# Optimization experiments

Measured on AMD Instinct MI355X. Metric: run time of the kernel, lower is better.

The kernel has to match this reference:

```python
import jax, jax.numpy as jnp
import numpy as np

EPS_L2 = 1e-6
EPS_RMS = 1e-6

def _dw_causal(x, w):
    # depthwise causal conv: x [B,L,C], w [C,K] (torch Conv1d weight [C,1,K] squeezed)
    K = w.shape[1]
    L = x.shape[1]
    xp = jnp.pad(x, ((0, 0), (K - 1, 0), (0, 0)))
    out = jnp.zeros_like(x)
    for j in range(K):  # K=4, fixed small kernel
        out = out + w[:, j] * xp[:, j:j + L, :]
    return out

def _qkv_conv(x, dw, pw):
    # depthwise causal conv -> pointwise 1x1 conv -> SiLU
    return jax.nn.silu(_dw_causal(x, dw) @ pw.T)

def _l2n(x):
    return x / (jnp.linalg.norm(x, axis=-1, keepdims=True) + EPS_L2)

def setup_inputs() -> dict:
    key = jax.random.key(0)
    B, L, D, M, P, K = 2, 1024, 2048, 2048, 8, 4
    ks = jax.random.split(key, 16)
    inp = {}
    inp['x'] = jax.random.normal(ks[0], (B, L, D), dtype=jnp.float32)
    inp['Wq'] = jax.random.normal(ks[1], (M, D), dtype=jnp.float32) * 0.02
    inp['Wk'] = jax.random.normal(ks[2], (M, D), dtype=jnp.float32) * 0.02
    inp['Wv'] = jax.random.normal(ks[3], (M, D), dtype=jnp.float32) * 0.02
    inp['q_dw'] = jax.random.normal(ks[4], (M, K), dtype=jnp.float32) * 0.1
    inp['k_dw'] = jax.random.normal(ks[5], (M, K), dtype=jnp.float32) * 0.1
    inp['v_dw'] = jax.random.normal(ks[6], (M, K), dtype=jnp.float32) * 0.1
    inp['q_pw'] = jax.random.normal(ks[7], (M, M), dtype=jnp.float32) * 0.02
    inp['k_pw'] = jax.random.normal(ks[8], (M, M), dtype=jnp.float32) * 0.02
    inp['v_pw'] = jax.random.normal(ks[9], (M, M), dtype=jnp.float32) * 0.02
    inp['pk'] = jax.random.normal(ks[10], (P, M), dtype=jnp.float32) * 0.02
    inp['pv'] = jax.random.normal(ks[11], (P, M), dtype=jnp.float32) * 0.02
    inp['mlp_w1'] = jnp.eye(M, dtype=jnp.float32) * 0.1
    inp['mlp_w2'] = jnp.eye(M, dtype=jnp.float32) * 0.1
    inp['eta_w'] = jnp.zeros((1, D), dtype=jnp.float32)
    inp['eta_b'] = jnp.full((1,), 2.0, dtype=jnp.float32)
    inp['theta_w'] = jnp.zeros((1, D), dtype=jnp.float32)
    inp['theta_b'] = jnp.full((1,), -1.0, dtype=jnp.float32)
    inp['alpha_w'] = jnp.zeros((1, D), dtype=jnp.float32)
    inp['alpha_b'] = jnp.full((1,), -2.0, dtype=jnp.float32)
    inp['gate_w'] = jax.random.normal(ks[12], (M, M), dtype=jnp.float32) * 0.02
    inp['gate_b'] = jnp.zeros((M,), dtype=jnp.float32)
    inp['out_w'] = jax.random.normal(ks[13], (D, M), dtype=jnp.float32) * 0.02
    inp['ln_w'] = jnp.ones((D,), dtype=jnp.float32)
    inp['mem_state'] = jnp.zeros((M, M), dtype=jnp.float32)
    inp['sur_state'] = jnp.zeros((M, M), dtype=jnp.float32)
    return inp

def reference(x, Wq, Wk, Wv, q_dw, q_pw, k_dw, k_pw, v_dw, v_pw, pk, pv,
              mlp_w1, mlp_w2, eta_w, eta_b, theta_w, theta_b, alpha_w, alpha_b,
              gate_w, gate_b, out_w, ln_w, mem_state, sur_state):
    B, L, D = x.shape
    M = Wq.shape[0]
    P = pk.shape[0]
    # projections + causal depthwise-separable convs + SiLU
    q = _qkv_conv(x @ Wq.T, q_dw, q_pw)
    k = _qkv_conv(x @ Wk.T, k_dw, k_pw)
    v = _qkv_conv(x @ Wv.T, v_dw, v_pw)
    q = _l2n(q)
    k = _l2n(k)
    # data-dependent eta/theta/alpha from mean-pooled input, scalarized
    x_pooled = x.mean(axis=1)  # [B, D]
    eta = jax.nn.sigmoid(x_pooled @ eta_w.T + eta_b).mean()
    theta = jax.nn.sigmoid(x_pooled @ theta_w.T + theta_b).mean()
    alpha = jax.nn.sigmoid(x_pooled @ alpha_w.T + alpha_b).mean()
    # persistent memory tokens
    pk_n = _l2n(pk)
    k_wp = jnp.concatenate([jnp.broadcast_to(pk_n[None], (B, P, M)), k], axis=1)
    v_wp = jnp.concatenate([jnp.broadcast_to(pv[None], (B, P, M)), v], axis=1)
    # test-time memory update (torch.no_grad block -> stop_gradient)
    pred = jnp.einsum('blm,mh->blh', k, mem_state)
    err = v - pred
    momentary = jnp.einsum('bld,blh->dh', k, err) / (B * L)
    new_surprise = eta * sur_state + theta * momentary
    new_memory = (1.0 - alpha) * mem_state + new_surprise
    snapshot = jax.lax.stop_gradient(new_memory)
    # retrieval: linear memory + deep memory MLP
    linear_ret = jnp.einsum('blm,mh->blh', q, snapshot)
    mlp_ret = jax.nn.silu(q @ mlp_w1.T) @ mlp_w2.T
    retrieved = linear_ret + mlp_ret
    # causal attention with always-visible persistent tokens
    scores = jnp.einsum('blm,bpm->blp', q, k_wp) / jnp.sqrt(jnp.float32(M))
    col = jnp.arange(P + L)
    row = jnp.arange(L)
    mask = (col[None, :] < P) | ((col[None, :] - P) <= row[:, None])  # [L, P+L]
    scores = jnp.where(mask[None], scores, -jnp.inf)
    attn = jax.nn.softmax(scores.astype(jnp.float32), axis=-1).astype(x.dtype)
    context = jnp.einsum('blp,bpm->blm', attn, v_wp)
    retrieved = retrieved + context
    # gated output projection + residual + RMSNorm
    gate = jax.nn.sigmoid(retrieved @ gate_w.T + gate_b)
    out = x + (gate * retrieved) @ out_w.T
    rms = jnp.sqrt(jnp.mean(out * out, axis=-1, keepdims=True) + EPS_RMS)
    return (out / rms) * ln_w
```

## Files before the change

### kernel.cpp

```cpp
#include <hip/hip_runtime.h>
#include <hip/hip_bf16.h>


#define NROWS 2048
#define MD    2048
#define PL    1032
#define PLP   1152
#define NM    4194304

using bf16x8 = __attribute__((ext_vector_type(8))) __bf16;
using f32x4  = __attribute__((ext_vector_type(4))) float;
using u16x8  = __attribute__((ext_vector_type(8))) unsigned short;

__device__ __forceinline__ unsigned short f2bf(float f) {
    union { float f; unsigned int u; } c; c.f = f;
    unsigned int u = c.u;
    return (unsigned short)((u + 0x7fffu + ((u >> 16) & 1u)) >> 16);
}
__device__ __forceinline__ float bf2f(unsigned short h) {
    union { float f; unsigned int u; } c; c.u = ((unsigned int)h) << 16;
    return c.f;
}
__device__ __forceinline__ float ldf(const float* p) { return *p; }
__device__ __forceinline__ float ldf(const unsigned short* p) { return bf2f(*p); }
__device__ __forceinline__ float sigm(float x) { return 1.f / (1.f + __expf(-x)); }
__device__ __forceinline__ float silu(float x) { return x / (1.f + __expf(-x)); }

__device__ __forceinline__ float block_reduce_sum(float v) {
    __shared__ float ws[4];
    #pragma unroll
    for (int o = 32; o > 0; o >>= 1) v += __shfl_down(v, o);
    __syncthreads();
    if ((threadIdx.x & 63) == 0) ws[threadIdx.x >> 6] = v;
    __syncthreads();
    return (ws[0] + ws[1]) + (ws[2] + ws[3]);
}
__device__ __forceinline__ float block_reduce_max(float v) {
    __shared__ float wm[4];
    #pragma unroll
    for (int o = 32; o > 0; o >>= 1) v = fmaxf(v, __shfl_down(v, o));
    __syncthreads();
    if ((threadIdx.x & 63) == 0) wm[threadIdx.x >> 6] = v;
    __syncthreads();
    return fmaxf(fmaxf(wm[0], wm[1]), fmaxf(wm[2], wm[3]));
}

__device__ __forceinline__ void load_lds16(const unsigned short* g, unsigned short* l) {
    __builtin_amdgcn_global_load_lds(
        (const __attribute__((address_space(1))) unsigned int*)g,
        (__attribute__((address_space(3))) unsigned int*)l, 16, 0, 0);
}
__device__ __forceinline__ void raw_barrier() {
    __asm__ volatile("" ::: "memory");
    __builtin_amdgcn_s_barrier();
    __asm__ volatile("" ::: "memory");
}
__device__ __forceinline__ void swz_bid(int& bx, int& by, int& bz) {
    const int gx = gridDim.x, gy = gridDim.y, gz = gridDim.z;
    const int nwg = gx * gy * gz;
    int id = blockIdx.x + gx * (blockIdx.y + gy * blockIdx.z);
    if ((nwg & 7) == 0) { int c = nwg >> 3; id = (id & 7) * c + (id >> 3); }
    bx = id % gx; id /= gx; by = id % gy; bz = id / gy;
}
__device__ __forceinline__ void epi_store(int epi, float* Cf, unsigned short* Ch,
                                          long off, int gc, float v,
                                          const float* gbp, const float* r1z,
                                          const float* r2z, unsigned short* qhz) {
    if (epi == 0)      Cf[off] = v;
    else if (epi == 1) Cf[off] += v;
    else if (epi == 2) Ch[off] = f2bf(v);
    else if (epi == 3) Ch[off] = f2bf(silu(v));
    else if (epi == 4) Ch[off] = f2bf(sigm(v + gbp[gc]) * (r1z[off] + r2z[off]));
    else { float r = Cf[off] + v; Cf[off] = r; qhz[off] = f2bf(r + r2z[off]); }
}

__global__ __launch_bounds__(256) void gemm_nt(
    const unsigned short* __restrict__ A, const unsigned short* __restrict__ Bm,
    void* __restrict__ Cv, int Mc, int K, long sA, long sB, long sCb, int epiPack,
    const float* __restrict__ gbp, const float* __restrict__ r1,
    const float* __restrict__ r2, unsigned short* __restrict__ qh)
{
    __shared__ unsigned short As[2][8192];
    __shared__ unsigned short Bs[2][4096];
    int bxx, byy, bzz; swz_bid(bxx, byy, bzz);
    const int tid = threadIdx.x, lane = tid & 63, w = tid >> 6;
    const int l16 = lane & 15, quad = lane >> 4;
    const int wr = (w >> 1) * 64, wc = (w & 1) * 32;
    const long rowBase = (long)byy * 128;
    const long colBase = (long)bxx * 64;
    const unsigned short* Ap = A + (long)bzz * sA;
    const unsigned short* Bp = Bm + (long)bzz * sB;
    const int epi = (epiPack >> (bzz * 4)) & 15;
    const int r8 = lane >> 3;
    const int cg = (lane & 7) ^ r8;

    const unsigned short* gA[4]; const unsigned short* gB[2];
    unsigned short* lA[4]; unsigned short* lB[2];
    #pragma unroll
    for (int t = 0; t < 4; ++t) {
        int ch = w * 4 + t;
        gA[t] = Ap + (rowBase + ch * 8 + r8) * (long)K + cg * 8;
        lA[t] = &As[0][ch * 512];
    }
    #pragma unroll
    for (int t = 0; t < 2; ++t) {
        int ch = w * 2 + t;
        gB[t] = Bp + (colBase + ch * 8 + r8) * (long)K + cg * 8;
        lB[t] = &Bs[0][ch * 512];
    }

    f32x4 acc[4][2] = {};
    #pragma unroll
    for (int t = 0; t < 4; ++t) { load_lds16(gA[t], lA[t]); gA[t] += 64; }
    #pragma unroll
    for (int t = 0; t < 2; ++t) { load_lds16(gB[t], lB[t]); gB[t] += 64; }

    const int nIter = K >> 6;
    for (int it = 0; it < nIter; ++it) {
        const int cb = it & 1;
        if (it + 1 < nIter) {
            const int nb = cb ^ 1;
            #pragma unroll
            for (int t = 0; t < 4; ++t) { load_lds16(gA[t], lA[t] + nb * 8192); gA[t] += 64; }
            #pragma unroll
            for (int t = 0; t < 2; ++t) { load_lds16(gB[t], lB[t] + nb * 4096); gB[t] += 64; }
            __builtin_amdgcn_s_waitcnt(0xF76);
        } else {
            __builtin_amdgcn_s_waitcnt(0xF70);
        }
        raw_barrier();
        const unsigned short* Ac = As[cb];
        const unsigned short* Bc = Bs[cb];
        #pragma unroll
        for (int ks = 0; ks < 2; ++ks) {
            const int cl = ((ks * 4 + quad) ^ (l16 & 7)) * 8;
            bf16x8 af[4], bfr[2];
            #pragma unroll
            for (int i = 0; i < 4; ++i)
                af[i] = *(const bf16x8*)&Ac[(wr + i * 16 + l16) * 64 + cl];
            #pragma unroll
            for (int j = 0; j < 2; ++j)
                bfr[j] = *(const bf16x8*)&Bc[(wc + j * 16 + l16) * 64 + cl];
            #pragma unroll
            for (int i = 0; i < 4; ++i)
                #pragma unroll
                for (int j = 0; j < 2; ++j)
                    acc[i][j] = __builtin_amdgcn_mfma_f32_16x16x32_bf16(af[i], bfr[j], acc[i][j], 0, 0, 0);
        }
        raw_barrier();
    }

    char* Cb = (char*)Cv + (long)bzz * sCb;
    float* Cf = (float*)Cb;
    unsigned short* Ch = (unsigned short*)Cb;
    const long zel = (long)bzz * (sCb >> 2);
    const float* r1z = r1 + zel;
    const float* r2z = r2 + zel;
    unsigned short* qhz = qh + zel;
    #pragma unroll
    for (int i = 0; i < 4; ++i)
        #pragma unroll
        for (int r = 0; r < 4; ++r) {
            long gr = rowBase + wr + i * 16 + quad * 4 + r;
            #pragma unroll
            for (int j = 0; j < 2; ++j) {
                long gc = colBase + wc + j * 16 + l16;
                epi_store(epi, Cf, Ch, gr * (long)Mc + gc, (int)gc, acc[i][j][r],
                          gbp, r1z, r2z, qhz);
            }
        }
}

#define P8_RD_A(p)                                                              \
    _Pragma("unroll") for (int fr = 0; fr < 2; ++fr)                            \
    _Pragma("unroll") for (int ks = 0; ks < 2; ++ks)                            \
        af[fr][ks] = *(const bf16x8*)&Ac[(wr + ((p) * 2 + fr) * 16 + l16) * 64  \
                                         + ((ks * 4 + quad) ^ (l16 & 7)) * 8];
#define P8_MFMA(p)                                                              \
    __builtin_amdgcn_s_setprio(1);                                              \
    _Pragma("unroll") for (int ks = 0; ks < 2; ++ks)                            \
    _Pragma("unroll") for (int fr = 0; fr < 2; ++fr)                            \
    _Pragma("unroll") for (int fc = 0; fc < FC; ++fc)                           \
        acc[(p) * 2 + fr][fc] = __builtin_amdgcn_mfma_f32_16x16x32_bf16(        \
            af[fr][ks], bfr[fc][ks], acc[(p) * 2 + fr][fc], 0, 0, 0);           \
    __builtin_amdgcn_s_setprio(0);
#define P8_STG_A(h)                                                             \
    do { load_lds16(gA[h][0], &Anx[lofsA[h][0]]); gA[h][0] += 64;               \
         load_lds16(gA[h][1], &Anx[lofsA[h][1]]); gA[h][1] += 64; } while (0)
#define P8_STG_B(j)                                                             \
    do { load_lds16(gB[j], &Bnx[lofsB[j]]); gB[j] += 64; } while (0)

template <int BN>
__global__ __launch_bounds__(512, 2) void gemm_nt_8p(
    const unsigned short* __restrict__ A, const unsigned short* __restrict__ Bm,
    void* __restrict__ Cv, int Mc, int K, long sA, long sB, long sCb, int epiPack,
    const unsigned short* __restrict__ rh)
{
    constexpr int LB = BN / 64;
    constexpr int FC = BN / 64;
    constexpr int WN = BN / 4;
    __shared__ unsigned short As[2][16384];
    __shared__ unsigned short Bs[2][BN * 64];
    int bx, by, bz; swz_bid(bx, by, bz);
    const int tid = threadIdx.x, lane = tid & 63, w = tid >> 6;
    const int l16 = lane & 15, quad = lane >> 4;
    const int wr = (w >> 2) * 128, wc = (w & 3) * WN;
    const long rowBase = (long)by * 256;
    const long colBase = (long)bx * BN;
    const unsigned short* Ap = A + (long)bz * sA;
    const unsigned short* Bp = Bm + (long)bz * sB;
    const int epi = (epiPack >> (bz * 4)) & 15;
    const int r8 = lane >> 3;
    const int cg = (lane & 7) ^ r8;

    const unsigned short* gA[2][2];
    int lofsA[2][2];
    #pragma unroll
    for (int h = 0; h < 2; ++h)
        #pragma unroll
        for (int j = 0; j < 2; ++j) {
            const int rowOff = h * 128 + j * 64 + w * 8 + r8;
            gA[h][j] = Ap + (rowBase + rowOff) * (long)K + cg * 8;
            lofsA[h][j] = (h * 128 + j * 64 + w * 8) * 64;
        }
    const unsigned short* gB[LB];
    int lofsB[LB];
    #pragma unroll
    for (int j = 0; j < LB; ++j) {
        const int rowOff = j * 64 + w * 8 + r8;
        gB[j] = Bp + (colBase + rowOff) * (long)K + cg * 8;
        lofsB[j] = (j * 64 + w * 8) * 64;
    }

    const int nT = K >> 6;
    f32x4 acc[8][FC] = {};

    #pragma unroll
    for (int h = 0; h < 2; ++h)
        #pragma unroll
        for (int j = 0; j < 2; ++j) { load_lds16(gA[h][j], &As[0][lofsA[h][j]]); gA[h][j] += 64; }
    #pragma unroll
    for (int j = 0; j < LB; ++j) { load_lds16(gB[j], &Bs[0][lofsB[j]]); gB[j] += 64; }
    if (nT > 1) {
        #pragma unroll
        for (int j = 0; j < LB; ++j) { load_lds16(gB[j], &Bs[1][lofsB[j]]); gB[j] += 64; }
        __builtin_amdgcn_s_waitcnt(0x0F70 | LB);
    } else {
        __builtin_amdgcn_s_waitcnt(0x0F70);
    }
    raw_barrier();

    for (int t = 0; t < nT; ++t) {
        const int cb = t & 1;
        const unsigned short* Ac = As[cb];
        const unsigned short* Bc = Bs[cb];
        unsigned short* Anx = As[cb ^ 1];
        unsigned short* Bnx = Bs[cb];
        const bool stA = (t + 1 < nT);
        const bool stB = (t + 2 < nT);
        bf16x8 bfr[FC][2];
        bf16x8 af[2][2];

        #pragma unroll
        for (int fc = 0; fc < FC; ++fc)
            #pragma unroll
            for (int ks = 0; ks < 2; ++ks)
                bfr[fc][ks] = *(const bf16x8*)&Bc[(wc + fc * 16 + l16) * 64
                                                 + ((ks * 4 + quad) ^ (l16 & 7)) * 8];
        P8_RD_A(0)
        if (stA) P8_STG_A(0);
        raw_barrier();
        P8_MFMA(0)
        raw_barrier();

        P8_RD_A(1)
        if (stA) P8_STG_A(1);
        raw_barrier();
        P8_MFMA(1)
        raw_barrier();

        P8_RD_A(2)
        if (stB) {
            #pragma unroll
            for (int j = 0; j < (LB + 1) / 2; ++j) P8_STG_B(j);
        }
        raw_barrier();
        P8_MFMA(2)
        raw_barrier();

        P8_RD_A(3)
        if (stB) {
            #pragma unroll
            for (int j = (LB + 1) / 2; j < LB; ++j) P8_STG_B(j);
            __builtin_amdgcn_s_waitcnt(0x0F70 | LB);
        } else {
            __builtin_amdgcn_s_waitcnt(0x0F70);
        }
        raw_barrier();
        P8_MFMA(3)
        raw_barrier();
    }

    char* Cb = (char*)Cv + (long)bz * sCb;
    float* Cf = (float*)Cb;
    unsigned short* Ch = (unsigned short*)Cb;
    #pragma unroll
    for (int i = 0; i < 8; ++i)
        #pragma unroll
        for (int r = 0; r < 4; ++r) {
            long gr = rowBase + wr + i * 16 + quad * 4 + r;
            #pragma unroll
            for (int j = 0; j < FC; ++j) {
                long gc = colBase + wc + j * 16 + l16;
                long off = gr * (long)Mc + gc;
                float v = acc[i][j][r];
                if (epi == 0)      Cf[off] = v;
                else if (epi == 2) Ch[off] = f2bf(v);
                else if (epi == 3) Ch[off] = f2bf(silu(v));
                else               Ch[off] = f2bf(bf2f(rh[off]) - v);
            }
        }
}

template <typename TS>
__global__ void k_transpose(const TS* __restrict__ src, unsigned short* __restrict__ dst,
                            int R, int C, int dstLd, int dstOff, long sSrc, long sDst)
{
    __shared__ float tile[32][33];
    const TS* sp = src + (long)blockIdx.z * sSrc;
    unsigned short* dp = dst + (long)blockIdx.z * sDst;
    int c0 = blockIdx.x * 32, r0 = blockIdx.y * 32;
    int tx = threadIdx.x, ty = threadIdx.y;
    #pragma unroll
    for (int i = 0; i < 4; ++i)
        tile[ty + i * 8][tx] = ldf(&sp[(long)(r0 + ty + i * 8) * C + c0 + tx]);
    __syncthreads();
    #pragma unroll
    for (int i = 0; i < 4; ++i)
        dp[(long)(c0 + ty + i * 8) * dstLd + dstOff + r0 + tx] = f2bf(tile[tx][ty + i * 8]);
}

__global__ void k_errT_kT(const unsigned short* __restrict__ errN,
                          const unsigned short* __restrict__ k_bf, unsigned short* __restrict__ eT)
{
    __shared__ float tile[32][33];
    int z = blockIdx.z;
    const unsigned short* src = (z == 0) ? errN : k_bf;
    int c0 = blockIdx.x * 32, r0 = blockIdx.y * 32;
    int tx = threadIdx.x, ty = threadIdx.y;
    #pragma unroll
    for (int i = 0; i < 4; ++i) {
        long idx = (long)(r0 + ty + i * 8) * MD + c0 + tx;
        tile[ty + i * 8][tx] = bf2f(src[idx]);
    }
    __syncthreads();
    unsigned short* dst = eT + (long)z * NM;
    #pragma unroll
    for (int i = 0; i < 4; ++i)
        dst[(long)(c0 + ty + i * 8) * MD + r0 + tx] = f2bf(tile[tx][ty + i * 8]);
}

__global__ void k_snapT(const float* __restrict__ mem, const float* __restrict__ sur,
                        const float* __restrict__ momT, const float* __restrict__ scal,
                        unsigned short* __restrict__ dst)
{
    __shared__ float tile[32][33];
    float eta = scal[0], theta = scal[1], alpha = scal[2];
    int h0 = blockIdx.y * 32, d0 = blockIdx.x * 32;
    int tx = threadIdx.x, ty = threadIdx.y;
    #pragma unroll
    for (int i = 0; i < 4; ++i) {
        long idx = (long)(d0 + ty + i * 8) * MD + h0 + tx;
        tile[ty + i * 8][tx] = (1.f - alpha) * mem[idx] + eta * sur[idx];
    }
    __syncthreads();
    #pragma unroll
    for (int i = 0; i < 4; ++i) {
        long oidx = (long)(h0 + ty + i * 8) * MD + d0 + tx;
        dst[oidx] = f2bf(tile[tx][ty + i * 8] + theta * (1.f / 2048.f) * momT[oidx]);
    }
}

__global__ void k_cvt_multi(const float* s0, const float* s1, const float* s2, const float* s3,
                            const float* s4, const float* s5, const float* s6, const float* s7,
                            unsigned short* d0, unsigned short* d1, unsigned short* d2, unsigned short* d3,
                            unsigned short* d4, unsigned short* d5, unsigned short* d6, unsigned short* d7)
{
    int seg = blockIdx.x >> 11;
    const float* s; unsigned short* d;
    switch (seg) {
        case 0: s = s0; d = d0; break;  case 1: s = s1; d = d1; break;
        case 2: s = s2; d = d2; break;  case 3: s = s3; d = d3; break;
        case 4: s = s4; d = d4; break;  case 5: s = s5; d = d5; break;
        case 6: s = s6; d = d6; break;  default: s = s7; d = d7; break;
    }
    long idx = ((long)(blockIdx.x & 2047) * 256 + threadIdx.x) * 8;
    float4 a = *(const float4*)(s + idx);
    float4 b = *(const float4*)(s + idx + 4);
    u16x8 o;
    o[0] = f2bf(a.x); o[1] = f2bf(a.y); o[2] = f2bf(a.z); o[3] = f2bf(a.w);
    o[4] = f2bf(b.x); o[5] = f2bf(b.y); o[6] = f2bf(b.z); o[7] = f2bf(b.w);
    *(u16x8*)(d + idx) = o;
}

__global__ void k_dwconv(const unsigned short* __restrict__ tproj,
                         const float* __restrict__ qdw, const float* __restrict__ kdw,
                         const float* __restrict__ vdw, unsigned short* __restrict__ conv)
{
    long u = (long)blockIdx.x * 256 + threadIdx.x;
    long flat = u * 8;
    int z = (int)(flat >> 22);
    int rem = (int)(flat & (NM - 1));
    int n = rem >> 11, m = rem & 2047;
    int l = n & 1023;
    const float* dw = (z == 0) ? qdw : (z == 1) ? kdw : vdw;
    const unsigned short* src = tproj + (long)n * 6144 + z * 2048 + m;
    float4 dwv[8];
    #pragma unroll
    for (int e = 0; e < 8; ++e) dwv[e] = *(const float4*)(dw + (m + e) * 4);
    float acc[8] = {};
    #pragma unroll
    for (int j = 0; j < 4; ++j) {
        int dl = j - 3;
        if (l + dl >= 0) {
            u16x8 r = *(const u16x8*)(src + (long)dl * 6144);
            #pragma unroll
            for (int e = 0; e < 8; ++e)
                acc[e] += ((const float*)&dwv[e])[j] * bf2f(r[e]);
        }
    }
    u16x8 o;
    #pragma unroll
    for (int e = 0; e < 8; ++e) o[e] = f2bf(acc[e]);
    *(u16x8*)(conv + (long)z * NM + (long)n * 2048 + m) = o;
}

__global__ void k_post_qkv(const unsigned short* __restrict__ tbf, unsigned short* __restrict__ q_bf,
                           unsigned short* __restrict__ k_bf, unsigned short* __restrict__ kwp)
{
    int bid = blockIdx.x, z = bid >> 11, n = bid & 2047;
    const unsigned short* row = tbf + (long)z * NM + (long)n * 2048;
    int t = threadIdx.x;
    u16x8 iv = *(const u16x8*)(row + t * 8);
    float v[8];
    #pragma unroll
    for (int e = 0; e < 8; ++e) v[e] = bf2f(iv[e]);
    float ss = 0.f;
    #pragma unroll
    for (int e = 0; e < 8; ++e) ss += v[e] * v[e];
    ss = block_reduce_sum(ss);
    float inv = 1.f / (sqrtf(ss) + 1e-6f);
    u16x8 o;
    #pragma unroll
    for (int e = 0; e < 8; ++e) o[e] = f2bf(v[e] * inv);
    if (z == 0) {
        *(u16x8*)(q_bf + (long)n * 2048 + t * 8) = o;
    } else {
        *(u16x8*)(k_bf + (long)n * 2048 + t * 8) = o;
        int bb = n >> 10, l = n & 1023;
        *(u16x8*)(kwp + ((long)bb * PLP + 8 + l) * MD + t * 8) = o;
    }
}

__global__ void k_misc(const float* __restrict__ pk, const float* __restrict__ pv,
                       unsigned short* __restrict__ kwp, unsigned short* __restrict__ vwpT)
{
    int bid = blockIdx.x, t = threadIdx.x;
    if (bid < 8) {
        const float* row = pk + bid * MD;
        float4 a = *(const float4*)(row + t * 8);
        float4 b = *(const float4*)(row + t * 8 + 4);
        float v[8] = {a.x, a.y, a.z, a.w, b.x, b.y, b.z, b.w};
        float ss = 0.f;
        #pragma unroll
        for (int e = 0; e < 8; ++e) ss += v[e] * v[e];
        ss = block_reduce_sum(ss);
        float inv = 1.f / (sqrtf(ss) + 1e-6f);
        u16x8 o;
        #pragma unroll
        for (int e = 0; e < 8; ++e) o[e] = f2bf(v[e] * inv);
        *(u16x8*)(kwp + (long)bid * MD + t * 8) = o;
        *(u16x8*)(kwp + (long)PLP * MD + (long)bid * MD + t * 8) = o;
    } else if (bid < 72) {
        int i = (bid - 8) * 256 + t;
        int m = i >> 3, pp = i & 7;
        unsigned short h = f2bf(pv[pp * MD + m]);
        vwpT[(long)m * PLP + pp] = h;
        vwpT[(long)MD * PLP + (long)m * PLP + pp] = h;
    } else if (bid < 312) {
        long flat = ((long)(bid - 72) * 256 + t) * 8;
        int b = (int)(flat / 245760);
        int r = (int)(flat % 245760);
        int j = 1032 + (r >> 11), m = r & 2047;
        u16x8 zz = {};
        *(u16x8*)(kwp + ((long)b * PLP + j) * MD + m) = zz;
    } else {
        long flat = ((long)(bid - 312) * 256 + t) * 8;
        int bm = (int)(flat / 120);
        int o = (int)(flat % 120);
        u16x8 zz = {};
        *(u16x8*)(vwpT + (long)bm * PLP + 1032 + o) = zz;
    }
}

__global__ void k_pooled(const float* __restrict__ x, const float* __restrict__ ew,
                         const float* __restrict__ tw, const float* __restrict__ aw,
                         float* __restrict__ dots, unsigned short* __restrict__ xbf) {
    int b = blockIdx.y;
    long flat = ((long)blockIdx.x * 256 + threadIdx.x) * 8;
    long gi = (long)b * 1024 * MD + flat;
    int d = (int)(flat & (MD - 1));
    float4 a = *(const float4*)(x + gi);
    float4 b4 = *(const float4*)(x + gi + 4);
    float xv[8] = {a.x, a.y, a.z, a.w, b4.x, b4.y, b4.z, b4.w};
    float4 e0 = *(const float4*)(ew + d), e1 = *(const float4*)(ew + d + 4);
    float4 t0 = *(const float4*)(tw + d), t1 = *(const float4*)(tw + d + 4);
    float4 w0 = *(const float4*)(aw + d), w1 = *(const float4*)(aw + d + 4);
    u16x8 o;
    #pragma unroll
    for (int e = 0; e < 8; ++e) o[e] = f2bf(xv[e]);
    *(u16x8*)(xbf + gi) = o;
    float s0 = xv[0]*e0.x + xv[1]*e0.y + xv[2]*e0.z + xv[3]*e0.w
             + xv[4]*e1.x + xv[5]*e1.y + xv[6]*e1.z + xv[7]*e1.w;
    float s1 = xv[0]*t0.x + xv[1]*t0.y + xv[2]*t0.z + xv[3]*t0.w
             + xv[4]*t1.x + xv[5]*t1.y + xv[6]*t1.z + xv[7]*t1.w;
    float s2 = xv[0]*w0.x + xv[1]*w0.y + xv[2]*w0.z + xv[3]*w0.w
             + xv[4]*w1.x + xv[5]*w1.y + xv[6]*w1.z + xv[7]*w1.w;
    s0 = block_reduce_sum(s0);
    if (threadIdx.x == 0) atomicAdd(&dots[0 + b], s0);
    s1 = block_reduce_sum(s1);
    if (threadIdx.x == 0) atomicAdd(&dots[2 + b], s1);
    s2 = block_reduce_sum(s2);
    if (threadIdx.x == 0) atomicAdd(&dots[4 + b], s2);
}
__global__ void k_scal_fin(const float* __restrict__ dots, const float* __restrict__ eb,
                           const float* __restrict__ tb, const float* __restrict__ ab,
                           float* __restrict__ scal) {
    if (threadIdx.x == 0 && blockIdx.x == 0) {
        const float invL = 1.f / 1024.f;
        float e = 0, th = 0, al = 0;
        for (int b = 0; b < 2; ++b) {
            e  += sigm(dots[0 + b] * invL + eb[0]);
            th += sigm(dots[2 + b] * invL + tb[0]);
            al += sigm(dots[4 + b] * invL + ab[0]);
        }
        scal[0] = e * 0.5f; scal[1] = th * 0.5f; scal[2] = al * 0.5f;
    }
}

__global__ void k_softmax(const float* __restrict__ S, unsigned short* __restrict__ attn) {
    int l = blockIdx.x, b = blockIdx.y;
    long base = ((long)b * 1024 + l) * PLP;
    int nvis = 8 + l + 1;
    const float scale = 0.022097086912079608f;
    int t = threadIdx.x;
    float vals[5];
    float mx = -1e30f;
    #pragma unroll
    for (int s = 0; s < 5; ++s) {
        int j = t + s * 256;
        float v = -1e30f;
        if (j < nvis) v = S[base + j] * scale;
        vals[s] = v;
        mx = fmaxf(mx, v);
    }
    mx = block_reduce_max(mx);
    float sum = 0.f;
    #pragma unroll
    for (int s = 0; s < 5; ++s) {
        int j = t + s * 256;
        float e = 0.f;
        if (j < nvis) e = __expf(vals[s] - mx);
        vals[s] = e; sum += e;
    }
    sum = block_reduce_sum(sum);
    float inv = 1.f / sum;
    #pragma unroll
    for (int s = 0; s < 5; ++s) {
        int j = t + s * 256;
        if (j < PLP) attn[base + j] = f2bf(vals[s] * inv);
    }
}

__global__ void k_final(const float* __restrict__ x, const float* __restrict__ y,
                        const float* __restrict__ lnw, float* __restrict__ out) {
    int n = blockIdx.x;
    long base = (long)n * MD;
    int t = threadIdx.x;
    float4 a0 = *(const float4*)(x + base + t * 8), a1 = *(const float4*)(x + base + t * 8 + 4);
    float4 b0 = *(const float4*)(y + base + t * 8), b1 = *(const float4*)(y + base + t * 8 + 4);
    float v[8] = {a0.x + b0.x, a0.y + b0.y, a0.z + b0.z, a0.w + b0.w,
                  a1.x + b1.x, a1.y + b1.y, a1.z + b1.z, a1.w + b1.w};
    float ss = 0.f;
    #pragma unroll
    for (int e = 0; e < 8; ++e) ss += v[e] * v[e];
    ss = block_reduce_sum(ss);
    float inv = rsqrtf(ss * (1.f / 2048.f) + 1e-6f);
    float4 w0 = *(const float4*)(lnw + t * 8), w1 = *(const float4*)(lnw + t * 8 + 4);
    float4 o0 = {v[0] * inv * w0.x, v[1] * inv * w0.y, v[2] * inv * w0.z, v[3] * inv * w0.w};
    float4 o1 = {v[4] * inv * w1.x, v[5] * inv * w1.y, v[6] * inv * w1.z, v[7] * inv * w1.w};
    *(float4*)(out + base + t * 8) = o0;
    *(float4*)(out + base + t * 8 + 4) = o1;
}

static inline void gemm64(hipStream_t st, const void* A, const void* B, void* C,
                          int Mc, int K, long sA, long sB, long sCb,
                          int gx, int gy, int gz, int epiPack,
                          const float* gbp = nullptr, const float* r1 = nullptr,
                          const float* r2 = nullptr, unsigned short* qh = nullptr) {
    hipLaunchKernelGGL(gemm_nt, dim3(gx, gy, gz), dim3(256), 0, st,
                       (const unsigned short*)A, (const unsigned short*)B, C,
                       Mc, K, sA, sB, sCb, epiPack, gbp, r1, r2, qh);
}
template <int BN>
static inline void gemm8p(hipStream_t st, const void* A, const void* B, void* C,
                          int Mc, int K, long sA, long sB, long sCb,
                          int gx, int gy, int gz, int epiPack,
                          const unsigned short* rh = nullptr) {
    hipLaunchKernelGGL(gemm_nt_8p<BN>, dim3(gx, gy, gz), dim3(512), 0, st,
                       (const unsigned short*)A, (const unsigned short*)B, C,
                       Mc, K, sA, sB, sCb, epiPack, rh);
}

extern "C" void kernel_launch(void* const* d_in, const int* in_sizes, int n_in,
                              void* d_out, int out_size, void* d_ws, size_t ws_size,
                              hipStream_t stream) {
    const float* x    = (const float*)d_in[0];
    const float* Wq   = (const float*)d_in[1];
    const float* Wk   = (const float*)d_in[2];
    const float* Wv   = (const float*)d_in[3];
    const float* qdw  = (const float*)d_in[4];
    const float* kdw  = (const float*)d_in[5];
    const float* vdw  = (const float*)d_in[6];
    const float* qpw  = (const float*)d_in[7];
    const float* kpw  = (const float*)d_in[8];
    const float* vpw  = (const float*)d_in[9];
    const float* pk   = (const float*)d_in[10];
    const float* pv   = (const float*)d_in[11];
    const float* mw1  = (const float*)d_in[12];
    const float* mw2  = (const float*)d_in[13];
    const float* etaw = (const float*)d_in[14];
    const float* etab = (const float*)d_in[15];
    const float* thw  = (const float*)d_in[16];
    const float* thb  = (const float*)d_in[17];
    const float* alw  = (const float*)d_in[18];
    const float* alb  = (const float*)d_in[19];
    const float* gw   = (const float*)d_in[20];
    const float* gb   = (const float*)d_in[21];
    const float* ow   = (const float*)d_in[22];
    const float* lnw  = (const float*)d_in[23];
    const float* mem  = (const float*)d_in[24];
    const float* sur  = (const float*)d_in[25];
    float* out = (float*)d_out;

    char* ws = (char*)d_ws;
    const size_t MB = 1024 * 1024;
    float* dots = (float*)ws;
    float* scal = (float*)(ws + 1024);
    float*          t0f  = (float*)(ws + 4096);
    float*          t1f  = t0f + NM;
    float*          t2f  = t0f + 2 * NM;
    unsigned short* tproj = (unsigned short*)t0f;
    unsigned short* t_bf  = (unsigned short*)t0f;
    unsigned short* vf    = t_bf + 2 * (long)NM;
    float*          retf = (float*)(ws + 4096 + 48 * MB);
    unsigned short* k_bf = (unsigned short*)(ws + 4096 + 64 * MB);
    unsigned short* q_bf = k_bf + NM;
    unsigned short* qc   = k_bf + 2 * NM;
    unsigned short* g_bf = k_bf;
    unsigned short* x_bf = (unsigned short*)(ws + 4096 + 88 * MB);
    unsigned short* errN = x_bf;
    unsigned short* attn = x_bf;
    unsigned short* wQKV = (unsigned short*)(ws + 4096 + 96 * MB);
    unsigned short* conv = wQKV;
    unsigned short* kwp  = wQKV;
    unsigned short* vwpT = kwp + (long)2 * PLP * MD;
    unsigned short* wPW  = (unsigned short*)(ws + 4096 + 120 * MB);
    unsigned short* eT   = wPW;
    unsigned short* kT   = eT + NM;
    unsigned short* gw_bf = wPW;
    unsigned short* ow_bf = wPW + NM;
    unsigned short* wMem  = (unsigned short*)(ws + 4096 + 144 * MB);
    unsigned short* wMlp1 = wMem + NM;
    unsigned short* wSnap = wMem;
    unsigned short* wMlp2 = wMem + NM;

    const dim3 b256(256);
    const dim3 bT(32, 8);

    hipMemsetAsync(dots, 0, 256, stream);
    hipLaunchKernelGGL(k_pooled, dim3(1024, 2), b256, 0, stream, x, etaw, thw, alw, dots, x_bf);
    hipLaunchKernelGGL(k_scal_fin, dim3(1), dim3(64), 0, stream, dots, etab, thb, alb, scal);
    hipLaunchKernelGGL(k_cvt_multi, dim3(14336), b256, 0, stream,
                       Wq, Wk, Wv, qpw, kpw, vpw, mw1, mw1,
                       wQKV, wQKV + NM, wQKV + 2 * (long)NM,
                       wPW, wPW + NM, wPW + 2 * (long)NM, wMlp1, wMlp1);
    hipLaunchKernelGGL(k_transpose<float>, dim3(64, 64, 1), bT, 0, stream,
                       mem, wMem, MD, MD, MD, 0, 0L, 0L);
    gemm8p<192>(stream, x_bf, wQKV, tproj, 6144, MD, 0, 0, 0, 32, 8, 1, 0x2);
    hipLaunchKernelGGL(k_dwconv, dim3(6144), b256, 0, stream, tproj, qdw, kdw, vdw, conv);
    gemm8p<256>(stream, conv, wPW, t_bf, MD, MD, NM, NM, (long)NM * 2, 8, 8, 3, 0x333);
    hipLaunchKernelGGL(k_misc, dim3(552), b256, 0, stream, pk, pv, kwp, vwpT);
    hipLaunchKernelGGL(k_post_qkv, dim3(4096), b256, 0, stream, t_bf, q_bf, k_bf, kwp);
    hipLaunchKernelGGL(k_transpose<unsigned short>, dim3(64, 32, 2), bT, 0, stream,
                       vf, vwpT, 1024, MD, PLP, 8, (long)1024 * MD, (long)MD * PLP);
    gemm8p<128>(stream, k_bf, wMem, errN, MD, MD, NM, NM,
                (long)((char*)qc - (char*)errN), 16, 8, 2, 0x37, vf);
    hipLaunchKernelGGL(k_errT_kT, dim3(64, 64, 2), bT, 0, stream, errN, k_bf, eT);
    gemm64(stream, eT, kT, t2f, MD, MD, 0, 0, 0, 32, 16, 1, 0);
    hipLaunchKernelGGL(k_snapT, dim3(64, 64), bT, 0, stream, mem, sur, t2f, scal, wSnap);
    hipLaunchKernelGGL(k_cvt_multi, dim3(6144), b256, 0, stream,
                       mw2, gw, ow, mw2, mw2, mw2, mw2, mw2,
                       wMlp2, gw_bf, ow_bf, wMlp2, wMlp2, wMlp2, wMlp2, wMlp2);
    gemm8p<128>(stream, q_bf, wSnap, retf, MD, MD, NM, NM,
                (long)((char*)t1f - (char*)retf), 16, 8, 2, 0x00);
    gemm64(stream, q_bf, kwp, t2f, PLP, MD,
           (long)1024 * MD, (long)PLP * MD, (long)1024 * PLP * 4, 18, 8, 2, 0);
    hipLaunchKernelGGL(k_softmax, dim3(1024, 2), b256, 0, stream, t2f, attn);
    gemm64(stream, attn, vwpT, retf, MD, PLP,
           (long)1024 * PLP, (long)MD * PLP, (long)1024 * MD * 4, 32, 8, 2, 0x55,
           nullptr, retf, t1f, qc);
    gemm64(stream, qc, gw_bf, g_bf, MD, MD, 0, 0, 0, 32, 16, 1, 4,
           gb, retf, t1f, nullptr);
    gemm64(stream, g_bf, ow_bf, t0f, MD, MD, 0, 0, 0, 32, 16, 1, 0);
    hipLaunchKernelGGL(k_final, dim3(2048), b256, 0, stream, x, t0f, lnw, out);
}
```

Baseline: 860.4 us.

## Add 128x128 double-buffered GEMM, retune QKV tile, replace pooled atomics with partials

Adds a new 128x128-tile bf16 MFMA GEMM kernel with double-buffered LDS loads and a simple epilogue. It replaces the 8-phase GEMM for the error and snapshot-retrieval GEMMs, which use M=2048 at 16x16x2 grids. The QKV projection switches from a 192-wide to a 256-wide tile variant with a 24-column grid. The pooled-dot kernel now loops over more elements per block and writes per-block partials, reduced in a 256-thread finalize kernel, removing the memset and atomics. The simpler GEMM may lose the overlap and priority scheduling of the existing pipelined kernel.

```diff
diff --git a/kernel.cpp b/kernel.cpp
--- a/kernel.cpp
+++ b/kernel.cpp
@@ -167,6 +167,98 @@
                 long gc = colBase + wc + j * 16 + l16;
                 epi_store(epi, Cf, Ch, gr * (long)Mc + gc, (int)gc, acc[i][j][r],
                           gbp, r1z, r2z, qhz);
+            }
+        }
+}
+
+__global__ __launch_bounds__(256) void gemm_nt_big(
+    const unsigned short* __restrict__ A, const unsigned short* __restrict__ Bm,
+    void* __restrict__ Cv, int Mc, int K, long sA, long sB, long sCb, int epiPack,
+    const unsigned short* __restrict__ rh)
+{
+    __shared__ unsigned short As[2][8192];
+    __shared__ unsigned short Bs[2][8192];
+    int bxx, byy, bzz; swz_bid(bxx, byy, bzz);
+    const int tid = threadIdx.x, lane = tid & 63, w = tid >> 6;
+    const int l16 = lane & 15, quad = lane >> 4;
+    const int wr = (w >> 1) * 64, wc = (w & 1) * 64;
+    const long rowBase = (long)byy * 128;
+    const long colBase = (long)bxx * 128;
+    const unsigned short* Ap = A + (long)bzz * sA;
+    const unsigned short* Bp = Bm + (long)bzz * sB;
+    const int epi = (epiPack >> (bzz * 4)) & 15;
+    const int r8 = lane >> 3;
+    const int cg = (lane & 7) ^ r8;
+
+    const unsigned short* gA[4]; const unsigned short* gB[4];
+    unsigned short* lA[4]; unsigned short* lB[4];
+    #pragma unroll
+    for (int t = 0; t < 4; ++t) {
+        int ch = w * 4 + t;
+        gA[t] = Ap + (rowBase + ch * 8 + r8) * (long)K + cg * 8;
+        lA[t] = &As[0][ch * 512];
+        gB[t] = Bp + (colBase + ch * 8 + r8) * (long)K + cg * 8;
+        lB[t] = &Bs[0][ch * 512];
+    }
+
+    f32x4 acc[4][4] = {};
+    #pragma unroll
+    for (int t = 0; t < 4; ++t) { load_lds16(gA[t], lA[t]); gA[t] += 64; }
+    #pragma unroll
+    for (int t = 0; t < 4; ++t) { load_lds16(gB[t], lB[t]); gB[t] += 64; }
+
+    const int nIter = K >> 6;
+    for (int it = 0; it < nIter; ++it) {
+        const int cb = it & 1;
+        if (it + 1 < nIter) {
+            const int nb = cb ^ 1;
+            #pragma unroll
+            for (int t = 0; t < 4; ++t) { load_lds16(gA[t], lA[t] + nb * 8192); gA[t] += 64; }
+            #pragma unroll
+            for (int t = 0; t < 4; ++t) { load_lds16(gB[t], lB[t] + nb * 8192); gB[t] += 64; }
+            __builtin_amdgcn_s_waitcnt(0xF78);
+        } else {
+            __builtin_amdgcn_s_waitcnt(0xF70);
+        }
+        raw_barrier();
+        const unsigned short* Ac = As[cb];
+        const unsigned short* Bc = Bs[cb];
+        #pragma unroll
+        for (int ks = 0; ks < 2; ++ks) {
+            const int cl = ((ks * 4 + quad) ^ (l16 & 7)) * 8;
+            bf16x8 af[4], bfr[4];
+            #pragma unroll
+            for (int i = 0; i < 4; ++i)
+                af[i] = *(const bf16x8*)&Ac[(wr + i * 16 + l16) * 64 + cl];
+            #pragma unroll
+            for (int j = 0; j < 4; ++j)
+                bfr[j] = *(const bf16x8*)&Bc[(wc + j * 16 + l16) * 64 + cl];
+            #pragma unroll
+            for (int i = 0; i < 4; ++i)
+                #pragma unroll
+                for (int j = 0; j < 4; ++j)
+                    acc[i][j] = __builtin_amdgcn_mfma_f32_16x16x32_bf16(af[i], bfr[j], acc[i][j], 0, 0, 0);
+        }
+        raw_barrier();
+    }
+
+    char* Cb = (char*)Cv + (long)bzz * sCb;
+    float* Cf = (float*)Cb;
+    unsigned short* Ch = (unsigned short*)Cb;
+    #pragma unroll
+    for (int i = 0; i < 4; ++i)
+        #pragma unroll
+        for (int r = 0; r < 4; ++r) {
+            long gr = rowBase + wr + i * 16 + quad * 4 + r;
+            #pragma unroll
+            for (int j = 0; j < 4; ++j) {
+                long gc = colBase + wc + j * 16 + l16;
+                long off = gr * (long)Mc + gc;
+                float v = acc[i][j][r];
+                if (epi == 0)      Cf[off] = v;
+                else if (epi == 2) Ch[off] = f2bf(v);
+                else if (epi == 3) Ch[off] = f2bf(silu(v));
+                else               Ch[off] = f2bf(bf2f(rh[off]) - v);
             }
         }
 }
@@ -505,46 +597,61 @@
 
 __global__ void k_pooled(const float* __restrict__ x, const float* __restrict__ ew,
                          const float* __restrict__ tw, const float* __restrict__ aw,
-                         float* __restrict__ dots, unsigned short* __restrict__ xbf) {
+                         float* __restrict__ part, unsigned short* __restrict__ xbf) {
     int b = blockIdx.y;
-    long flat = ((long)blockIdx.x * 256 + threadIdx.x) * 8;
-    long gi = (long)b * 1024 * MD + flat;
-    int d = (int)(flat & (MD - 1));
-    float4 a = *(const float4*)(x + gi);
-    float4 b4 = *(const float4*)(x + gi + 4);
-    float xv[8] = {a.x, a.y, a.z, a.w, b4.x, b4.y, b4.z, b4.w};
-    float4 e0 = *(const float4*)(ew + d), e1 = *(const float4*)(ew + d + 4);
-    float4 t0 = *(const float4*)(tw + d), t1 = *(const float4*)(tw + d + 4);
-    float4 w0 = *(const float4*)(aw + d), w1 = *(const float4*)(aw + d + 4);
-    u16x8 o;
-    #pragma unroll
-    for (int e = 0; e < 8; ++e) o[e] = f2bf(xv[e]);
-    *(u16x8*)(xbf + gi) = o;
-    float s0 = xv[0]*e0.x + xv[1]*e0.y + xv[2]*e0.z + xv[3]*e0.w
-             + xv[4]*e1.x + xv[5]*e1.y + xv[6]*e1.z + xv[7]*e1.w;
-    float s1 = xv[0]*t0.x + xv[1]*t0.y + xv[2]*t0.z + xv[3]*t0.w
-             + xv[4]*t1.x + xv[5]*t1.y + xv[6]*t1.z + xv[7]*t1.w;
-    float s2 = xv[0]*w0.x + xv[1]*w0.y + xv[2]*w0.z + xv[3]*w0.w
-             + xv[4]*w1.x + xv[5]*w1.y + xv[6]*w1.z + xv[7]*w1.w;
+    long base = (long)b * 1024 * MD;
+    long start = (long)blockIdx.x * 16384;
+    float s0 = 0.f, s1 = 0.f, s2 = 0.f;
+    #pragma unroll
+    for (int s = 0; s < 8; ++s) {
+        long flat = start + ((long)s * 256 + threadIdx.x) * 8;
+        long gi = base + flat;
+        int d = (int)(flat & (MD - 1));
+        float4 a = *(const float4*)(x + gi);
+        float4 b4 = *(const float4*)(x + gi + 4);
+        float xv[8] = {a.x, a.y, a.z, a.w, b4.x, b4.y, b4.z, b4.w};
+        u16x8 o;
+        #pragma unroll
+        for (int e = 0; e < 8; ++e) o[e] = f2bf(xv[e]);
+        *(u16x8*)(xbf + gi) = o;
+        float4 e0 = *(const float4*)(ew + d), e1 = *(const float4*)(ew + d + 4);
+        float4 t0 = *(const float4*)(tw + d), t1 = *(const float4*)(tw + d + 4);
+        float4 w0 = *(const float4*)(aw + d), w1 = *(const float4*)(aw + d + 4);
+        s0 += xv[0]*e0.x + xv[1]*e0.y + xv[2]*e0.z + xv[3]*e0.w
+            + xv[4]*e1.x + xv[5]*e1.y + xv[6]*e1.z + xv[7]*e1.w;
+        s1 += xv[0]*t0.x + xv[1]*t0.y + xv[2]*t0.z + xv[3]*t0.w
+            + xv[4]*t1.x + xv[5]*t1.y + xv[6]*t1.z + xv[7]*t1.w;
+        s2 += xv[0]*w0.x + xv[1]*w0.y + xv[2]*w0.z + xv[3]*w0.w
+            + xv[4]*w1.x + xv[5]*w1.y + xv[6]*w1.z + xv[7]*w1.w;
+    }
     s0 = block_reduce_sum(s0);
-    if (threadIdx.x == 0) atomicAdd(&dots[0 + b], s0);
+    if (threadIdx.x == 0) part[0 * 256 + b * 128 + blockIdx.x] = s0;
     s1 = block_reduce_sum(s1);
-    if (threadIdx.x == 0) atomicAdd(&dots[2 + b], s1);
+    if (threadIdx.x == 0) part[1 * 256 + b * 128 + blockIdx.x] = s1;
     s2 = block_reduce_sum(s2);
-    if (threadIdx.x == 0) atomicAdd(&dots[4 + b], s2);
-}
-__global__ void k_scal_fin(const float* __restrict__ dots, const float* __restrict__ eb,
+    if (threadIdx.x == 0) part[2 * 256 + b * 128 + blockIdx.x] = s2;
+}
+__global__ void k_scal_fin(const float* __restrict__ part, const float* __restrict__ eb,
                            const float* __restrict__ tb, const float* __restrict__ ab,
                            float* __restrict__ scal) {
-    if (threadIdx.x == 0 && blockIdx.x == 0) {
+    int t = threadIdx.x;
+    float v[6];
+    #pragma unroll
+    for (int c = 0; c < 3; ++c)
+        #pragma unroll
+        for (int b = 0; b < 2; ++b)
+            v[c * 2 + b] = (t < 128) ? part[c * 256 + b * 128 + t] : 0.f;
+    float d00 = block_reduce_sum(v[0]);
+    float d01 = block_reduce_sum(v[1]);
+    float d10 = block_reduce_sum(v[2]);
+    float d11 = block_reduce_sum(v[3]);
+    float d20 = block_reduce_sum(v[4]);
+    float d21 = block_reduce_sum(v[5]);
+    if (t == 0) {
         const float invL = 1.f / 1024.f;
-        float e = 0, th = 0, al = 0;
-        for (int b = 0; b < 2; ++b) {
-            e  += sigm(dots[0 + b] * invL + eb[0]);
-            th += sigm(dots[2 + b] * invL + tb[0]);
-            al += sigm(dots[4 + b] * invL + ab[0]);
-        }
-        scal[0] = e * 0.5f; scal[1] = th * 0.5f; scal[2] = al * 0.5f;
+        scal[0] = 0.5f * (sigm(d00 * invL + eb[0]) + sigm(d01 * invL + eb[0]));
+        scal[1] = 0.5f * (sigm(d10 * invL + tb[0]) + sigm(d11 * invL + tb[0]));
+        scal[2] = 0.5f * (sigm(d20 * invL + ab[0]) + sigm(d21 * invL + ab[0]));
     }
 }
 
@@ -611,6 +718,14 @@
     hipLaunchKernelGGL(gemm_nt, dim3(gx, gy, gz), dim3(256), 0, st,
                        (const unsigned short*)A, (const unsigned short*)B, C,
                        Mc, K, sA, sB, sCb, epiPack, gbp, r1, r2, qh);
+}
+static inline void gemm128(hipStream_t st, const void* A, const void* B, void* C,
+                           int Mc, int K, long sA, long sB, long sCb,
+                           int gx, int gy, int gz, int epiPack,
+                           const unsigned short* rh = nullptr) {
+    hipLaunchKernelGGL(gemm_nt_big, dim3(gx, gy, gz), dim3(256), 0, st,
+                       (const unsigned short*)A, (const unsigned short*)B, C,
+                       Mc, K, sA, sB, sCb, epiPack, rh);
 }
 template <int BN>
 static inline void gemm8p(hipStream_t st, const void* A, const void* B, void* C,
@@ -655,8 +770,8 @@
 
     char* ws = (char*)d_ws;
     const size_t MB = 1024 * 1024;
-    float* dots = (float*)ws;
-    float* scal = (float*)(ws + 1024);
+    float* part = (float*)ws;
+    float* scal = (float*)(ws + 3584);
     float*          t0f  = (float*)(ws + 4096);
     float*          t1f  = t0f + NM;
     float*          t2f  = t0f + 2 * NM;
@@ -688,32 +803,31 @@
     const dim3 b256(256);
     const dim3 bT(32, 8);
 
-    hipMemsetAsync(dots, 0, 256, stream);
-    hipLaunchKernelGGL(k_pooled, dim3(1024, 2), b256, 0, stream, x, etaw, thw, alw, dots, x_bf);
-    hipLaunchKernelGGL(k_scal_fin, dim3(1), dim3(64), 0, stream, dots, etab, thb, alb, scal);
+    hipLaunchKernelGGL(k_pooled, dim3(128, 2), b256, 0, stream, x, etaw, thw, alw, part, x_bf);
+    hipLaunchKernelGGL(k_scal_fin, dim3(1), b256, 0, stream, part, etab, thb, alb, scal);
     hipLaunchKernelGGL(k_cvt_multi, dim3(14336), b256, 0, stream,
                        Wq, Wk, Wv, qpw, kpw, vpw, mw1, mw1,
                        wQKV, wQKV + NM, wQKV + 2 * (long)NM,
                        wPW, wPW + NM, wPW + 2 * (long)NM, wMlp1, wMlp1);
     hipLaunchKernelGGL(k_transpose<float>, dim3(64, 64, 1), bT, 0, stream,
                        mem, wMem, MD, MD, MD, 0, 0L, 0L);
-    gemm8p<192>(stream, x_bf, wQKV, tproj, 6144, MD, 0, 0, 0, 32, 8, 1, 0x2);
+    gemm8p<256>(stream, x_bf, wQKV, tproj, 6144, MD, 0, 0, 0, 24, 8, 1, 0x2);
     hipLaunchKernelGGL(k_dwconv, dim3(6144), b256, 0, stream, tproj, qdw, kdw, vdw, conv);
     gemm8p<256>(stream, conv, wPW, t_bf, MD, MD, NM, NM, (long)NM * 2, 8, 8, 3, 0x333);
     hipLaunchKernelGGL(k_misc, dim3(552), b256, 0, stream, pk, pv, kwp, vwpT);
     hipLaunchKernelGGL(k_post_qkv, dim3(4096), b256, 0, stream, t_bf, q_bf, k_bf, kwp);
     hipLaunchKernelGGL(k_transpose<unsigned short>, dim3(64, 32, 2), bT, 0, stream,
                        vf, vwpT, 1024, MD, PLP, 8, (long)1024 * MD, (long)MD * PLP);
-    gemm8p<128>(stream, k_bf, wMem, errN, MD, MD, NM, NM,
-                (long)((char*)qc - (char*)errN), 16, 8, 2, 0x37, vf);
+    gemm128(stream, k_bf, wMem, errN, MD, MD, NM, NM,
+            (long)((char*)qc - (char*)errN), 16, 16, 2, 0x37, vf);
     hipLaunchKernelGGL(k_errT_kT, dim3(64, 64, 2), bT, 0, stream, errN, k_bf, eT);
     gemm64(stream, eT, kT, t2f, MD, MD, 0, 0, 0, 32, 16, 1, 0);
     hipLaunchKernelGGL(k_snapT, dim3(64, 64), bT, 0, stream, mem, sur, t2f, scal, wSnap);
     hipLaunchKernelGGL(k_cvt_multi, dim3(6144), b256, 0, stream,
                        mw2, gw, ow, mw2, mw2, mw2, mw2, mw2,
                        wMlp2, gw_bf, ow_bf, wMlp2, wMlp2, wMlp2, wMlp2, wMlp2);
-    gemm8p<128>(stream, q_bf, wSnap, retf, MD, MD, NM, NM,
-                (long)((char*)t1f - (char*)retf), 16, 8, 2, 0x00);
+    gemm128(stream, q_bf, wSnap, retf, MD, MD, NM, NM,
+            (long)((char*)t1f - (char*)retf), 16, 16, 2, 0x00);
     gemm64(stream, q_bf, kwp, t2f, PLP, MD,
            (long)1024 * MD, (long)PLP * MD, (long)1024 * PLP * 4, 18, 8, 2, 0);
     hipLaunchKernelGGL(k_softmax, dim3(1024, 2), b256, 0, stream, t2f, attn);
```

New measurement: 767.9 us. 10.7% less time.
